# Optimization experiments

Hardware: AMD Instinct MI355X
Metric: run time of the kernel (lower is better)

The kernel has to match this reference:

```python
import jax, jax.numpy as jnp
import numpy as np

N_E = 200000   # number of entities
N_T = 1000000  # number of KB triples
N_R = 200      # number of relations
N_W2V = 300    # question embedding dim
B = 64         # batch size


def _one_step(x, r, subj, rel, obj):
    # torch.sparse.mm(M_subj, x.T)      -> gather: x[:, subj]  (B, N_T)
    # torch.sparse.mm(M_rel.T, r.T)     -> gather: r[:, rel]   (B, N_T)
    # torch.sparse.mm(M_obj.T, x_t*r_t) -> scatter-add over obj ids
    m = x[:, subj] * r[:, rel]                                   # (B, N_T)
    x_new = jax.ops.segment_sum(m.T, obj, num_segments=N_E).T    # (B, N_E)
    return x_new


def setup_inputs() -> dict:
    key = jax.random.key(0)
    ks = jax.random.split(key, 11)
    x = jax.random.uniform(ks[0], (B, N_E), dtype=jnp.float32)
    q = jax.random.normal(ks[1], (B, N_W2V), dtype=jnp.float32)
    subj = jax.random.randint(ks[2], (N_T,), 0, N_E, dtype=jnp.int32)
    rel = jax.random.randint(ks[3], (N_T,), 0, N_R, dtype=jnp.int32)
    obj = jax.random.randint(ks[4], (N_T,), 0, N_E, dtype=jnp.int32)
    s = 1.0 / np.sqrt(N_W2V)  # nn.Linear default init scale
    W1 = jax.random.uniform(ks[5], (N_W2V, N_R), minval=-s, maxval=s, dtype=jnp.float32)
    b1 = jax.random.uniform(ks[6], (N_R,), minval=-s, maxval=s, dtype=jnp.float32)
    W2 = jax.random.uniform(ks[7], (N_W2V, N_R), minval=-s, maxval=s, dtype=jnp.float32)
    b2 = jax.random.uniform(ks[8], (N_R,), minval=-s, maxval=s, dtype=jnp.float32)
    W3 = jax.random.uniform(ks[9], (N_W2V, N_R), minval=-s, maxval=s, dtype=jnp.float32)
    b3 = jax.random.uniform(ks[10], (N_R,), minval=-s, maxval=s, dtype=jnp.float32)
    return {"x": x, "q": q, "W1": W1, "b1": b1, "W2": W2, "b2": b2,
            "W3": W3, "b3": b3, "subj": subj, "rel": rel, "obj": obj,
            "n_hop": 3}


def reference(x, q, W1, b1, W2, b2, W3, b3, subj, rel, obj, n_hop):
    layers = [(W1, b1), (W2, b2), (W3, b3)]
    for W, b in layers[:n_hop]:
        r = q @ W + b              # dense_i(q): (B, N_R)
        x = _one_step(x, r, subj, rel, obj)
    return x
```

## Files before the change

### kernel.cpp

```cpp
#include <hip/hip_runtime.h>
#include <hip/hip_fp16.h>

#define WAVE 64
#define NXCD 8
#define NRMAX 200
#define RSTRIDE 17
#define HOP_TPB 1024
#define HOP_BLOCKS 512
#define CSR_BLOCKS 2048
#define CSR_TPB 256
#define CAP 16
#define OVF_CAP 32768

typedef int v4i __attribute__((ext_vector_type(4)));


__global__ void prologue_kernel(const float* __restrict__ x, const float* __restrict__ q,
                                const float* __restrict__ W1, const float* __restrict__ b1,
                                const float* __restrict__ W2, const float* __restrict__ b2,
                                const float* __restrict__ W3, const float* __restrict__ b3,
                                float* __restrict__ rT, __half2* __restrict__ xT,
                                int* __restrict__ cnt, int N_E, int N_R, int N_W2V,
                                int tgrid, int nrx, int rblocks, int zcount) {
    __shared__ float tile[64][65];
    int bid = blockIdx.x;
    if (bid < tgrid) {
        int e0 = bid * 64;
        int li = threadIdx.x & 63;
        int lo = threadIdx.x >> 6;
        #pragma unroll
        for (int k = 0; k < 16; ++k) {
            int b = lo + 4 * k;
            int e = e0 + li;
            tile[b][li] = (e < N_E) ? x[(size_t)b * N_E + e] : 0.0f;
        }
        __syncthreads();
        #pragma unroll
        for (int k = 0; k < 8; ++k) {
            int idx = k * 256 + threadIdx.x;
            int ei  = idx >> 5;
            int j   = idx & 31;
            int e   = e0 + ei;
            if (e < N_E)
                xT[(size_t)e * 32 + j] = __floats2half2_rn(tile[2 * j][ei], tile[2 * j + 1][ei]);
        }
    } else if (bid < tgrid + rblocks) {
        int rb = bid - tgrid;
        int bx = rb % nrx;
        int by = rb / nrx;
        int lane = threadIdx.x & 63;
        int wv   = threadIdx.x >> 6;
        int b    = by * 4 + wv;
        int it   = bx * 64 + lane;
        if (it >= 3 * N_R) return;
        int l = it / N_R;
        int j = it - l * N_R;
        const float* W  = (l == 0) ? W1 : (l == 1) ? W2 : W3;
        const float* bv = (l == 0) ? b1 : (l == 1) ? b2 : b3;
        const float* qrow = q + (size_t)b * N_W2V;
        float a0 = 0.f, a1 = 0.f, a2 = 0.f, a3 = 0.f;
        int k = 0;
        for (; k + 4 <= N_W2V; k += 4) {
            a0 = fmaf(qrow[k + 0], W[(size_t)(k + 0) * N_R + j], a0);
            a1 = fmaf(qrow[k + 1], W[(size_t)(k + 1) * N_R + j], a1);
            a2 = fmaf(qrow[k + 2], W[(size_t)(k + 2) * N_R + j], a2);
            a3 = fmaf(qrow[k + 3], W[(size_t)(k + 3) * N_R + j], a3);
        }
        for (; k < N_W2V; ++k)
            a0 = fmaf(qrow[k], W[(size_t)k * N_R + j], a0);
        rT[(size_t)it * WAVE + b] = bv[j] + ((a0 + a1) + (a2 + a3));
    } else {
        int zb = bid - tgrid - rblocks;
        int i4 = zb * 256 + threadIdx.x;
        if (i4 < zcount) ((v4i*)cnt)[i4] = (v4i){0, 0, 0, 0};
    }
}


__global__ void scatter_direct_kernel(const int* __restrict__ subj, const int* __restrict__ rel,
                                      const int* __restrict__ obj,
                                      int* __restrict__ cnt, unsigned* __restrict__ slots,
                                      int* __restrict__ novf, int* __restrict__ ovf_obj,
                                      unsigned* __restrict__ ovf_pk, int nT, int nE) {
    int grp = blockIdx.x & (NXCD - 1);
    int sh  = (nE + NXCD - 1) / NXCD;
    int lo  = grp * sh;
    int hi  = min(nE, lo + sh);
    int tid    = (blockIdx.x >> 3) * blockDim.x + threadIdx.x;
    int stride = (gridDim.x >> 3) * blockDim.x;
    int nT4 = nT >> 2;
    const v4i* obj4 = (const v4i*)obj;
    for (int t = tid; t < nT4; t += stride) {
        v4i o = obj4[t];
        int base = t * 4;
        int  oo[4];
        bool mk[4];
        unsigned pk[4];
        int  slot[4];
        #pragma unroll
        for (int u = 0; u < 4; ++u) {
            oo[u] = o[u];
            mk[u] = (oo[u] >= lo && oo[u] < hi);
            pk[u] = mk[u] ? ((unsigned)subj[base + u] | ((unsigned)rel[base + u] << 18)) : 0u;
        }
        #pragma unroll
        for (int u = 0; u < 4; ++u)
            if (mk[u]) slot[u] = atomicAdd(&cnt[oo[u]], 1);
        #pragma unroll
        for (int u = 0; u < 4; ++u) {
            if (mk[u]) {
                if (slot[u] < CAP) slots[(size_t)oo[u] * CAP + slot[u]] = pk[u];
                else {
                    int oi = atomicAdd(novf, 1);
                    if (oi < OVF_CAP) { ovf_obj[oi] = oo[u]; ovf_pk[oi] = pk[u]; }
                }
            }
        }
    }
    for (int t = nT4 * 4 + tid; t < nT; t += stride) {
        int oo = obj[t];
        if (oo >= lo && oo < hi) {
            unsigned pk = (unsigned)subj[t] | ((unsigned)rel[t] << 18);
            int slot = atomicAdd(&cnt[oo], 1);
            if (slot < CAP) slots[(size_t)oo * CAP + slot] = pk;
            else {
                int oi = atomicAdd(novf, 1);
                if (oi < OVF_CAP) { ovf_obj[oi] = oo; ovf_pk[oi] = pk; }
            }
        }
    }
}


__device__ __forceinline__ float4 h4_to_f4(uint2 v) {
    float2 f0 = __half22float2(*(__half2*)&v.x);
    float2 f1 = __half22float2(*(__half2*)&v.y);
    return make_float4(f0.x, f0.y, f1.x, f1.y);
}

__device__ __forceinline__ uint2 pack_half4(float4 a) {
    __half2 h0 = __floats2half2_rn(a.x, a.y);
    __half2 h1 = __floats2half2_rn(a.z, a.w);
    uint2 v;
    v.x = *(unsigned*)&h0;
    v.y = *(unsigned*)&h1;
    return v;
}

__device__ __forceinline__ float4 hop_accum4(const uint2* __restrict__ xp,
                                             const float4* __restrict__ r_lds,
                                             const int* __restrict__ cnt,
                                             const unsigned* __restrict__ slots,
                                             int e, int g, int c, int nE) {
    float4 acc = make_float4(0.f, 0.f, 0.f, 0.f);
    int len = (e < nE) ? min(cnt[e], CAP) : 0;
    unsigned pv = (c < len) ? slots[(size_t)e * CAP + c] : 0u;
    int m = max(len, __shfl_xor(len, 16));
    m = max(m, __shfl_xor(m, 32));
    for (int j0 = 0; j0 < m; j0 += 8) {
        uint2 xv[8];
        unsigned pr[8];
        #pragma unroll
        for (int u = 0; u < 8; ++u) {
            int jj = max(min(j0 + u, len - 1), 0);
            unsigned p = __shfl(pv, (g << 4) + jj);
            pr[u] = p >> 18;
            xv[u] = xp[(size_t)(p & 0x3FFFFu) * 16 + c];
        }
        #pragma unroll
        for (int u = 0; u < 8; ++u) {
            if (j0 + u < len) {
                float4 rv = r_lds[pr[u] * RSTRIDE + c];
                float4 xf = h4_to_f4(xv[u]);
                acc.x = fmaf(xf.x, rv.x, acc.x);
                acc.y = fmaf(xf.y, rv.y, acc.y);
                acc.z = fmaf(xf.z, rv.z, acc.z);
                acc.w = fmaf(xf.w, rv.w, acc.w);
            }
        }
    }
    return acc;
}

__global__ __launch_bounds__(HOP_TPB, 8)
void hop_mid_kernel(const uint2* __restrict__ xp, const float4* __restrict__ rT4,
                    const int* __restrict__ cnt, const unsigned* __restrict__ slots,
                    uint2* __restrict__ yh, int nE, int nR) {
    __shared__ float4 r_lds[NRMAX * RSTRIDE];
    for (int i = threadIdx.x; i < nR * 16; i += HOP_TPB)
        r_lds[(i >> 4) * RSTRIDE + (i & 15)] = rT4[i];
    __syncthreads();
    int lane = threadIdx.x & 63;
    int g = lane >> 4, c = lane & 15;
    int wv = threadIdx.x >> 6;
    int nTiles = (nE + 63) >> 6;
    for (int t = blockIdx.x; t < nTiles; t += gridDim.x) {
        int e = t * 64 + wv * 4 + g;
        float4 acc = hop_accum4(xp, r_lds, cnt, slots, e, g, c, nE);
        if (e < nE) yh[(size_t)e * 16 + c] = pack_half4(acc);
    }
}

__global__ __launch_bounds__(HOP_TPB, 8)
void hop_out_kernel(const uint2* __restrict__ xp, const float4* __restrict__ rT4,
                    const int* __restrict__ cnt, const unsigned* __restrict__ slots,
                    float* __restrict__ out, int nE, int nR) {
    __shared__ float4 r_lds[NRMAX * RSTRIDE];
    __shared__ float tile[64][65];
    for (int i = threadIdx.x; i < nR * 16; i += HOP_TPB)
        r_lds[(i >> 4) * RSTRIDE + (i & 15)] = rT4[i];
    __syncthreads();
    int lane = threadIdx.x & 63;
    int g = lane >> 4, c = lane & 15;
    int wv = threadIdx.x >> 6;
    int nTiles = (nE + 63) >> 6;
    for (int t = blockIdx.x; t < nTiles; t += gridDim.x) {
        int e0 = t * 64;
        int ei = wv * 4 + g;
        float4 acc = hop_accum4(xp, r_lds, cnt, slots, e0 + ei, g, c, nE);
        tile[ei][4 * c + 0] = acc.x;
        tile[ei][4 * c + 1] = acc.y;
        tile[ei][4 * c + 2] = acc.z;
        tile[ei][4 * c + 3] = acc.w;
        __syncthreads();
        #pragma unroll
        for (int k = 0; k < 4; ++k) {
            int b = wv * 4 + k;
            int e = e0 + lane;
            if (e < nE) out[(size_t)b * nE + e] = tile[lane][b];
        }
        __syncthreads();
    }
}

__device__ __forceinline__ void atom_add_h2(unsigned* addr, float a, float b) {
    unsigned old = __atomic_load_n(addr, __ATOMIC_RELAXED), assumed;
    do {
        assumed = old;
        float2 f = __half22float2(*(__half2*)&assumed);
        __half2 nh = __floats2half2_rn(f.x + a, f.y + b);
        old = atomicCAS(addr, assumed, *(unsigned*)&nh);
    } while (old != assumed);
}

__global__ void ovf_mid_kernel(const uint2* __restrict__ xp, const float* __restrict__ rTl,
                               const int* __restrict__ novf, const int* __restrict__ ovf_obj,
                               const unsigned* __restrict__ ovf_pk, uint2* __restrict__ yh) {
    int n = min(*novf, OVF_CAP);
    int c = threadIdx.x & 15, grp = threadIdx.x >> 4;
    for (int i = blockIdx.x * 4 + grp; i < n; i += gridDim.x * 4) {
        int o = ovf_obj[i];
        unsigned p = ovf_pk[i];
        float4 xf = h4_to_f4(xp[(size_t)(p & 0x3FFFFu) * 16 + c]);
        const float* rr = rTl + (size_t)(p >> 18) * 64 + c * 4;
        unsigned* w = (unsigned*)&yh[(size_t)o * 16 + c];
        atom_add_h2(w,     xf.x * rr[0], xf.y * rr[1]);
        atom_add_h2(w + 1, xf.z * rr[2], xf.w * rr[3]);
    }
}

__global__ void ovf_out_kernel(const uint2* __restrict__ xp, const float* __restrict__ rTl,
                               const int* __restrict__ novf, const int* __restrict__ ovf_obj,
                               const unsigned* __restrict__ ovf_pk, float* __restrict__ out, int nE) {
    int n = min(*novf, OVF_CAP);
    int c = threadIdx.x & 15, grp = threadIdx.x >> 4;
    for (int i = blockIdx.x * 4 + grp; i < n; i += gridDim.x * 4) {
        int o = ovf_obj[i];
        unsigned p = ovf_pk[i];
        float4 xf = h4_to_f4(xp[(size_t)(p & 0x3FFFFu) * 16 + c]);
        const float* rr = rTl + (size_t)(p >> 18) * 64 + c * 4;
        atomicAdd(&out[(size_t)(4 * c + 0) * nE + o], xf.x * rr[0]);
        atomicAdd(&out[(size_t)(4 * c + 1) * nE + o], xf.y * rr[1]);
        atomicAdd(&out[(size_t)(4 * c + 2) * nE + o], xf.z * rr[2]);
        atomicAdd(&out[(size_t)(4 * c + 3) * nE + o], xf.w * rr[3]);
    }
}

extern "C" void kernel_launch(void* const* d_in, const int* in_sizes, int n_in,
                              void* d_out, int out_size, void* d_ws, size_t ws_size,
                              hipStream_t stream) {
    const float* x  = (const float*)d_in[0];
    const float* q  = (const float*)d_in[1];
    const float* W1 = (const float*)d_in[2];
    const float* b1 = (const float*)d_in[3];
    const float* W2 = (const float*)d_in[4];
    const float* b2 = (const float*)d_in[5];
    const float* W3 = (const float*)d_in[6];
    const float* b3 = (const float*)d_in[7];
    const int* subj = (const int*)d_in[8];
    const int* rel  = (const int*)d_in[9];
    const int* obj  = (const int*)d_in[10];

    const int B     = 64;
    const int N_E   = in_sizes[0] / B;
    const int N_W2V = in_sizes[1] / B;
    const int N_R   = in_sizes[3];
    const int N_T   = in_sizes[8];

    const size_t h16bytes = (size_t)N_E * B * sizeof(__half);

    int*      cnt     = (int*)d_ws;
    int*      novf    = cnt + N_E;
    int*      ovf_obj = novf + 4;
    unsigned* ovf_pk  = (unsigned*)(ovf_obj + OVF_CAP);
    unsigned* slots   = ovf_pk + OVF_CAP;
    char*     rT_raw  = (char*)(slots + (size_t)N_E * CAP);
    float*    rT      = (float*)(((uintptr_t)rT_raw + 15) & ~(uintptr_t)15);
    char*     X0      = (char*)(rT + (size_t)3 * N_R * B);
    size_t used = (size_t)(X0 - (char*)d_ws) + h16bytes;

    char* H1;
    if (ws_size >= used + h16bytes) {
        H1 = X0 + h16bytes;
        used += h16bytes;
    } else {
        H1 = (char*)d_out;
    }
    char* H2 = X0;

    int tgrid   = (N_E + 63) / 64;
    int nrx     = (3 * N_R + 63) / 64;
    int rblocks = nrx * (B / 4);
    int zcount  = (N_E + 4) / 4;
    int zblocks = (zcount + 255) / 256;
    prologue_kernel<<<tgrid + rblocks + zblocks, 256, 0, stream>>>(
        x, q, W1, b1, W2, b2, W3, b3, rT, (__half2*)X0, cnt,
        N_E, N_R, N_W2V, tgrid, nrx, rblocks, zcount);

    scatter_direct_kernel<<<CSR_BLOCKS, CSR_TPB, 0, stream>>>(
        subj, rel, obj, cnt, slots, novf, ovf_obj, ovf_pk, N_T, N_E);

    int hblocks = tgrid < HOP_BLOCKS ? tgrid : HOP_BLOCKS;
    const float* rT1 = rT;
    const float* rT2 = rT + (size_t)1 * N_R * B;
    const float* rT3 = rT + (size_t)2 * N_R * B;

    hop_mid_kernel<<<hblocks, HOP_TPB, 0, stream>>>(
        (const uint2*)X0, (const float4*)rT1, cnt, slots, (uint2*)H1, N_E, N_R);
    ovf_mid_kernel<<<16, 64, 0, stream>>>(
        (const uint2*)X0, rT1, novf, ovf_obj, ovf_pk, (uint2*)H1);

    hop_mid_kernel<<<hblocks, HOP_TPB, 0, stream>>>(
        (const uint2*)H1, (const float4*)rT2, cnt, slots, (uint2*)H2, N_E, N_R);
    ovf_mid_kernel<<<16, 64, 0, stream>>>(
        (const uint2*)H1, rT2, novf, ovf_obj, ovf_pk, (uint2*)H2);

    hop_out_kernel<<<hblocks, HOP_TPB, 0, stream>>>(
        (const uint2*)H2, (const float4*)rT3, cnt, slots, (float*)d_out, N_E, N_R);
    ovf_out_kernel<<<16, 64, 0, stream>>>(
        (const uint2*)H2, rT3, novf, ovf_obj, ovf_pk, (float*)d_out, N_E);
}
```

Baseline: 345.1 us.

## Fuse scatter and three hops into one cooperative persistent kernel

Replaces the scatter kernel, three hop kernels and three overflow kernels with a single cooperative kernel that uses grid-wide syncs between phases. Overflow triples are now handled inside the gather, where each overflowing entity scans the whole overflow list, instead of by separate atomic kernels. The aim is to remove six kernel launches and their inter-kernel gaps. In exchange, the scatter phase runs with fewer threads (at most 512 blocks), grid syncs add cost, and the overflow scan is linear per overflowing entity.

Result: slower. 962.7 us (+179.0%).

```diff
diff --git a/kernel.cpp b/kernel.cpp
--- a/kernel.cpp
+++ b/kernel.cpp
@@ -1,5 +1,8 @@
 #include <hip/hip_runtime.h>
 #include <hip/hip_fp16.h>
+#include <hip/hip_cooperative_groups.h>
+
+namespace cg = cooperative_groups;
 
 #define WAVE 64
 #define NXCD 8
@@ -7,13 +10,10 @@
 #define RSTRIDE 17
 #define HOP_TPB 1024
 #define HOP_BLOCKS 512
-#define CSR_BLOCKS 2048
-#define CSR_TPB 256
 #define CAP 16
 #define OVF_CAP 32768
 
 typedef int v4i __attribute__((ext_vector_type(4)));
-
 
 __global__ void prologue_kernel(const float* __restrict__ x, const float* __restrict__ q,
                                 const float* __restrict__ W1, const float* __restrict__ b1,
@@ -76,62 +76,6 @@
     }
 }
 
-
-__global__ void scatter_direct_kernel(const int* __restrict__ subj, const int* __restrict__ rel,
-                                      const int* __restrict__ obj,
-                                      int* __restrict__ cnt, unsigned* __restrict__ slots,
-                                      int* __restrict__ novf, int* __restrict__ ovf_obj,
-                                      unsigned* __restrict__ ovf_pk, int nT, int nE) {
-    int grp = blockIdx.x & (NXCD - 1);
-    int sh  = (nE + NXCD - 1) / NXCD;
-    int lo  = grp * sh;
-    int hi  = min(nE, lo + sh);
-    int tid    = (blockIdx.x >> 3) * blockDim.x + threadIdx.x;
-    int stride = (gridDim.x >> 3) * blockDim.x;
-    int nT4 = nT >> 2;
-    const v4i* obj4 = (const v4i*)obj;
-    for (int t = tid; t < nT4; t += stride) {
-        v4i o = obj4[t];
-        int base = t * 4;
-        int  oo[4];
-        bool mk[4];
-        unsigned pk[4];
-        int  slot[4];
-        #pragma unroll
-        for (int u = 0; u < 4; ++u) {
-            oo[u] = o[u];
-            mk[u] = (oo[u] >= lo && oo[u] < hi);
-            pk[u] = mk[u] ? ((unsigned)subj[base + u] | ((unsigned)rel[base + u] << 18)) : 0u;
-        }
-        #pragma unroll
-        for (int u = 0; u < 4; ++u)
-            if (mk[u]) slot[u] = atomicAdd(&cnt[oo[u]], 1);
-        #pragma unroll
-        for (int u = 0; u < 4; ++u) {
-            if (mk[u]) {
-                if (slot[u] < CAP) slots[(size_t)oo[u] * CAP + slot[u]] = pk[u];
-                else {
-                    int oi = atomicAdd(novf, 1);
-                    if (oi < OVF_CAP) { ovf_obj[oi] = oo[u]; ovf_pk[oi] = pk[u]; }
-                }
-            }
-        }
-    }
-    for (int t = nT4 * 4 + tid; t < nT; t += stride) {
-        int oo = obj[t];
-        if (oo >= lo && oo < hi) {
-            unsigned pk = (unsigned)subj[t] | ((unsigned)rel[t] << 18);
-            int slot = atomicAdd(&cnt[oo], 1);
-            if (slot < CAP) slots[(size_t)oo * CAP + slot] = pk;
-            else {
-                int oi = atomicAdd(novf, 1);
-                if (oi < OVF_CAP) { ovf_obj[oi] = oo; ovf_pk[oi] = pk; }
-            }
-        }
-    }
-}
-
-
 __device__ __forceinline__ float4 h4_to_f4(uint2 v) {
     float2 f0 = __half22float2(*(__half2*)&v.x);
     float2 f1 = __half22float2(*(__half2*)&v.y);
@@ -151,9 +95,13 @@
                                              const float4* __restrict__ r_lds,
                                              const int* __restrict__ cnt,
                                              const unsigned* __restrict__ slots,
+                                             const int* __restrict__ novf,
+                                             const int* __restrict__ ovf_obj,
+                                             const unsigned* __restrict__ ovf_pk,
                                              int e, int g, int c, int nE) {
     float4 acc = make_float4(0.f, 0.f, 0.f, 0.f);
-    int len = (e < nE) ? min(cnt[e], CAP) : 0;
+    int lraw = (e < nE) ? cnt[e] : 0;
+    int len = min(lraw, CAP);
     unsigned pv = (c < len) ? slots[(size_t)e * CAP + c] : 0u;
     int m = max(len, __shfl_xor(len, 16));
     m = max(m, __shfl_xor(m, 32));
@@ -179,45 +127,116 @@
             }
         }
     }
+    if (__any(lraw > CAP)) {
+        if (lraw > CAP) {
+            int n = min(*novf, OVF_CAP);
+            for (int i = 0; i < n; ++i) {
+                if (ovf_obj[i] == e) {
+                    unsigned p = ovf_pk[i];
+                    float4 xf = h4_to_f4(xp[(size_t)(p & 0x3FFFFu) * 16 + c]);
+                    float4 rv = r_lds[(p >> 18) * RSTRIDE + c];
+                    acc.x = fmaf(xf.x, rv.x, acc.x);
+                    acc.y = fmaf(xf.y, rv.y, acc.y);
+                    acc.z = fmaf(xf.z, rv.z, acc.z);
+                    acc.w = fmaf(xf.w, rv.w, acc.w);
+                }
+            }
+        }
+    }
     return acc;
 }
 
-__global__ __launch_bounds__(HOP_TPB, 8)
-void hop_mid_kernel(const uint2* __restrict__ xp, const float4* __restrict__ rT4,
-                    const int* __restrict__ cnt, const unsigned* __restrict__ slots,
-                    uint2* __restrict__ yh, int nE, int nR) {
-    __shared__ float4 r_lds[NRMAX * RSTRIDE];
+__device__ __forceinline__ void stage_r(const float4* __restrict__ rT4, int nR, float4* r_lds) {
     for (int i = threadIdx.x; i < nR * 16; i += HOP_TPB)
         r_lds[(i >> 4) * RSTRIDE + (i & 15)] = rT4[i];
     __syncthreads();
+}
+
+__global__ __launch_bounds__(HOP_TPB, 8)
+void mega_kernel(const int* __restrict__ subj, const int* __restrict__ rel,
+                 const int* __restrict__ obj,
+                 int* __restrict__ cnt, unsigned* __restrict__ slots,
+                 int* __restrict__ novf, int* __restrict__ ovf_obj, unsigned* __restrict__ ovf_pk,
+                 const uint2* __restrict__ X0, uint2* __restrict__ H1, uint2* __restrict__ H2,
+                 const float4* __restrict__ rT4, float* __restrict__ out,
+                 int nE, int nR, int nT) {
+    cg::grid_group grid = cg::this_grid();
+    __shared__ float4 r_lds[NRMAX * RSTRIDE];
+    __shared__ float tile[64][65];
+
+    {
+        int grp = blockIdx.x & (NXCD - 1);
+        int sh  = (nE + NXCD - 1) / NXCD;
+        int lo  = grp * sh;
+        int hi  = min(nE, lo + sh);
+        int tid    = (blockIdx.x >> 3) * blockDim.x + threadIdx.x;
+        int stride = (gridDim.x >> 3) * blockDim.x;
+        int nT4 = nT >> 2;
+        const v4i* obj4 = (const v4i*)obj;
+        for (int t = tid; t < nT4; t += stride) {
+            v4i o = obj4[t];
+            int base = t * 4;
+            #pragma unroll
+            for (int u = 0; u < 4; ++u) {
+                int oo = o[u];
+                if (oo >= lo && oo < hi) {
+                    unsigned pk = (unsigned)subj[base + u] | ((unsigned)rel[base + u] << 18);
+                    int slot = atomicAdd(&cnt[oo], 1);
+                    if (slot < CAP) slots[(size_t)oo * CAP + slot] = pk;
+                    else {
+                        int oi = atomicAdd(novf, 1);
+                        if (oi < OVF_CAP) { ovf_obj[oi] = oo; ovf_pk[oi] = pk; }
+                    }
+                }
+            }
+        }
+        for (int t = nT4 * 4 + tid; t < nT; t += stride) {
+            int oo = obj[t];
+            if (oo >= lo && oo < hi) {
+                unsigned pk = (unsigned)subj[t] | ((unsigned)rel[t] << 18);
+                int slot = atomicAdd(&cnt[oo], 1);
+                if (slot < CAP) slots[(size_t)oo * CAP + slot] = pk;
+                else {
+                    int oi = atomicAdd(novf, 1);
+                    if (oi < OVF_CAP) { ovf_obj[oi] = oo; ovf_pk[oi] = pk; }
+                }
+            }
+        }
+    }
+    __threadfence();
+    grid.sync();
+    __threadfence();
+
     int lane = threadIdx.x & 63;
     int g = lane >> 4, c = lane & 15;
     int wv = threadIdx.x >> 6;
     int nTiles = (nE + 63) >> 6;
+
+    stage_r(rT4, nR, r_lds);
     for (int t = blockIdx.x; t < nTiles; t += gridDim.x) {
         int e = t * 64 + wv * 4 + g;
-        float4 acc = hop_accum4(xp, r_lds, cnt, slots, e, g, c, nE);
-        if (e < nE) yh[(size_t)e * 16 + c] = pack_half4(acc);
-    }
-}
-
-__global__ __launch_bounds__(HOP_TPB, 8)
-void hop_out_kernel(const uint2* __restrict__ xp, const float4* __restrict__ rT4,
-                    const int* __restrict__ cnt, const unsigned* __restrict__ slots,
-                    float* __restrict__ out, int nE, int nR) {
-    __shared__ float4 r_lds[NRMAX * RSTRIDE];
-    __shared__ float tile[64][65];
-    for (int i = threadIdx.x; i < nR * 16; i += HOP_TPB)
-        r_lds[(i >> 4) * RSTRIDE + (i & 15)] = rT4[i];
-    __syncthreads();
-    int lane = threadIdx.x & 63;
-    int g = lane >> 4, c = lane & 15;
-    int wv = threadIdx.x >> 6;
-    int nTiles = (nE + 63) >> 6;
+        float4 acc = hop_accum4(X0, r_lds, cnt, slots, novf, ovf_obj, ovf_pk, e, g, c, nE);
+        if (e < nE) H1[(size_t)e * 16 + c] = pack_half4(acc);
+    }
+    __threadfence();
+    grid.sync();
+    __threadfence();
+
+    stage_r(rT4 + (size_t)nR * 16, nR, r_lds);
+    for (int t = blockIdx.x; t < nTiles; t += gridDim.x) {
+        int e = t * 64 + wv * 4 + g;
+        float4 acc = hop_accum4(H1, r_lds, cnt, slots, novf, ovf_obj, ovf_pk, e, g, c, nE);
+        if (e < nE) H2[(size_t)e * 16 + c] = pack_half4(acc);
+    }
+    __threadfence();
+    grid.sync();
+    __threadfence();
+
+    stage_r(rT4 + (size_t)2 * nR * 16, nR, r_lds);
     for (int t = blockIdx.x; t < nTiles; t += gridDim.x) {
         int e0 = t * 64;
         int ei = wv * 4 + g;
-        float4 acc = hop_accum4(xp, r_lds, cnt, slots, e0 + ei, g, c, nE);
+        float4 acc = hop_accum4(H2, r_lds, cnt, slots, novf, ovf_obj, ovf_pk, e0 + ei, g, c, nE);
         tile[ei][4 * c + 0] = acc.x;
         tile[ei][4 * c + 1] = acc.y;
         tile[ei][4 * c + 2] = acc.z;
@@ -230,49 +249,6 @@
             if (e < nE) out[(size_t)b * nE + e] = tile[lane][b];
         }
         __syncthreads();
-    }
-}
-
-__device__ __forceinline__ void atom_add_h2(unsigned* addr, float a, float b) {
-    unsigned old = __atomic_load_n(addr, __ATOMIC_RELAXED), assumed;
-    do {
-        assumed = old;
-        float2 f = __half22float2(*(__half2*)&assumed);
-        __half2 nh = __floats2half2_rn(f.x + a, f.y + b);
-        old = atomicCAS(addr, assumed, *(unsigned*)&nh);
-    } while (old != assumed);
-}
-
-__global__ void ovf_mid_kernel(const uint2* __restrict__ xp, const float* __restrict__ rTl,
-                               const int* __restrict__ novf, const int* __restrict__ ovf_obj,
-                               const unsigned* __restrict__ ovf_pk, uint2* __restrict__ yh) {
-    int n = min(*novf, OVF_CAP);
-    int c = threadIdx.x & 15, grp = threadIdx.x >> 4;
-    for (int i = blockIdx.x * 4 + grp; i < n; i += gridDim.x * 4) {
-        int o = ovf_obj[i];
-        unsigned p = ovf_pk[i];
-        float4 xf = h4_to_f4(xp[(size_t)(p & 0x3FFFFu) * 16 + c]);
-        const float* rr = rTl + (size_t)(p >> 18) * 64 + c * 4;
-        unsigned* w = (unsigned*)&yh[(size_t)o * 16 + c];
-        atom_add_h2(w,     xf.x * rr[0], xf.y * rr[1]);
-        atom_add_h2(w + 1, xf.z * rr[2], xf.w * rr[3]);
-    }
-}
-
-__global__ void ovf_out_kernel(const uint2* __restrict__ xp, const float* __restrict__ rTl,
-                               const int* __restrict__ novf, const int* __restrict__ ovf_obj,
-                               const unsigned* __restrict__ ovf_pk, float* __restrict__ out, int nE) {
-    int n = min(*novf, OVF_CAP);
-    int c = threadIdx.x & 15, grp = threadIdx.x >> 4;
-    for (int i = blockIdx.x * 4 + grp; i < n; i += gridDim.x * 4) {
-        int o = ovf_obj[i];
-        unsigned p = ovf_pk[i];
-        float4 xf = h4_to_f4(xp[(size_t)(p & 0x3FFFFu) * 16 + c]);
-        const float* rr = rTl + (size_t)(p >> 18) * 64 + c * 4;
-        atomicAdd(&out[(size_t)(4 * c + 0) * nE + o], xf.x * rr[0]);
-        atomicAdd(&out[(size_t)(4 * c + 1) * nE + o], xf.y * rr[1]);
-        atomicAdd(&out[(size_t)(4 * c + 2) * nE + o], xf.z * rr[2]);
-        atomicAdd(&out[(size_t)(4 * c + 3) * nE + o], xf.w * rr[3]);
     }
 }
 
@@ -327,26 +303,26 @@
         x, q, W1, b1, W2, b2, W3, b3, rT, (__half2*)X0, cnt,
         N_E, N_R, N_W2V, tgrid, nrx, rblocks, zcount);
 
-    scatter_direct_kernel<<<CSR_BLOCKS, CSR_TPB, 0, stream>>>(
-        subj, rel, obj, cnt, slots, novf, ovf_obj, ovf_pk, N_T, N_E);
-
-    int hblocks = tgrid < HOP_BLOCKS ? tgrid : HOP_BLOCKS;
-    const float* rT1 = rT;
-    const float* rT2 = rT + (size_t)1 * N_R * B;
-    const float* rT3 = rT + (size_t)2 * N_R * B;
-
-    hop_mid_kernel<<<hblocks, HOP_TPB, 0, stream>>>(
-        (const uint2*)X0, (const float4*)rT1, cnt, slots, (uint2*)H1, N_E, N_R);
-    ovf_mid_kernel<<<16, 64, 0, stream>>>(
-        (const uint2*)X0, rT1, novf, ovf_obj, ovf_pk, (uint2*)H1);
-
-    hop_mid_kernel<<<hblocks, HOP_TPB, 0, stream>>>(
-        (const uint2*)H1, (const float4*)rT2, cnt, slots, (uint2*)H2, N_E, N_R);
-    ovf_mid_kernel<<<16, 64, 0, stream>>>(
-        (const uint2*)H1, rT2, novf, ovf_obj, ovf_pk, (uint2*)H2);
-
-    hop_out_kernel<<<hblocks, HOP_TPB, 0, stream>>>(
-        (const uint2*)H2, (const float4*)rT3, cnt, slots, (float*)d_out, N_E, N_R);
-    ovf_out_kernel<<<16, 64, 0, stream>>>(
-        (const uint2*)H2, rT3, novf, ovf_obj, ovf_pk, (float*)d_out, N_E);
-}
+    int maxb = 0;
+    hipOccupancyMaxActiveBlocksPerMultiprocessor(&maxb, mega_kernel, HOP_TPB, 0);
+    if (maxb < 1) maxb = 1;
+    int mgrid = maxb * 256;
+    if (mgrid > HOP_BLOCKS) mgrid = HOP_BLOCKS;
+    mgrid &= ~7;
+    if (mgrid < 8) mgrid = 8;
+
+    const uint2*  X0u  = (const uint2*)X0;
+    uint2*        H1u  = (uint2*)H1;
+    uint2*        H2u  = (uint2*)H2;
+    const float4* rT4p = (const float4*)rT;
+    float*        outp = (float*)d_out;
+    int nE_ = N_E, nR_ = N_R, nT_ = N_T;
+    void* kargs[] = {
+        (void*)&subj, (void*)&rel, (void*)&obj,
+        (void*)&cnt, (void*)&slots, (void*)&novf, (void*)&ovf_obj, (void*)&ovf_pk,
+        (void*)&X0u, (void*)&H1u, (void*)&H2u, (void*)&rT4p, (void*)&outp,
+        (void*)&nE_, (void*)&nR_, (void*)&nT_
+    };
+    hipLaunchCooperativeKernel((void*)mega_kernel, dim3(mgrid), dim3(HOP_TPB),
+                               kargs, 0, stream);
+}
```
